# Kernel optimization log

Measured on AMD Instinct MI355X. Metric: run time of the kernel, lower is better.

## Reference

```python
import jax, jax.numpy as jnp
import numpy as np

N, D_IN, D_LAT, K = 200000, 256, 64, 100
ALPHA = 1000.0


def setup_inputs() -> dict:
    key = jax.random.key(0)
    k1, k2, k3, k4 = jax.random.split(key, 4)
    X = jax.random.normal(k1, (N, D_IN), dtype=jnp.float32)
    encoding = jax.random.normal(k2, (N, D_LAT), dtype=jnp.float32)
    decoding = jax.random.normal(k3, (N, D_IN), dtype=jnp.float32)
    # xavier_uniform bound for [K, D]: sqrt(6/(K+D))
    bound = np.sqrt(6.0 / (K + D_LAT)).astype(np.float32)
    centres = jax.random.uniform(k4, (K, D_LAT), dtype=jnp.float32,
                                 minval=-bound, maxval=bound)
    return {"X": X, "encoding": encoding, "decoding": decoding, "centres": centres}


def _cluster_kl(encoding, centres):
    # squared euclidean distances [N, K]
    d2 = (jnp.sum(encoding * encoding, axis=1, keepdims=True)
          + jnp.sum(centres * centres, axis=1)[None, :]
          - 2.0 * encoding @ centres.T)
    d2 = jnp.maximum(d2, 0.0)
    # Student-t (1 dof) soft assignment (DEC)
    q = 1.0 / (1.0 + d2)
    q = q / jnp.sum(q, axis=1, keepdims=True)          # [N, K]
    # target distribution p = (q^2 / f) normalized, detached
    f = jnp.sum(q, axis=0)                              # [K]
    p = (q * q) / f
    p = p / jnp.sum(p, axis=1, keepdims=True)
    p = jax.lax.stop_gradient(p)
    # F.kl_div(log q, p, reduction='batchmean') = sum p*(log p - log q) / N
    kl = jnp.sum(p * (jnp.log(p) - jnp.log(q))) / q.shape[0]
    return kl


def reference(X, encoding, decoding, centres):
    decoder_loss = jnp.mean((X - decoding) ** 2)
    cluster_loss = _cluster_kl(encoding, centres)
    return decoder_loss + cluster_loss * ALPHA
```

## Files before the change

### kernel.cpp

```cpp
#include <hip/hip_runtime.h>

#define N_ROWS 200000
#define D_IN   256
#define D_LAT  64
#define K_CL   100
#define NT     7
#define TPB    256

#define GRPS   3125
#define NMF    625
#define GPB    5

#define SC_HALF   3125
#define NSLOT     64

typedef __attribute__((ext_vector_type(8))) short bf16x8;
typedef __attribute__((ext_vector_type(4))) float f32x4;

__device__ __forceinline__ float rcpf(float x) { return __builtin_amdgcn_rcpf(x); }

__device__ __forceinline__ short f2bf(float f) {
    union { float f; unsigned u; } v; v.f = f;
    unsigned r = (v.u + 0x7fffu + ((v.u >> 16) & 1u)) >> 16;
    return (short)r;
}

__device__ __forceinline__ void cvt8r(float4 a, float4 b, bf16x8& o, float& sq) {
    sq = fmaf(a.x, a.x, sq); sq = fmaf(a.y, a.y, sq);
    sq = fmaf(a.z, a.z, sq); sq = fmaf(a.w, a.w, sq);
    sq = fmaf(b.x, b.x, sq); sq = fmaf(b.y, b.y, sq);
    sq = fmaf(b.z, b.z, sq); sq = fmaf(b.w, b.w, sq);
    o[0] = f2bf(a.x); o[1] = f2bf(a.y); o[2] = f2bf(a.z); o[3] = f2bf(a.w);
    o[4] = f2bf(b.x); o[5] = f2bf(b.y); o[6] = f2bf(b.z); o[7] = f2bf(b.w);
}

__device__ __forceinline__ void cvt8(const float* __restrict__ p, bf16x8& o, float& sq) {
    float4 a = *(const float4*)p;
    float4 b = *(const float4*)(p + 4);
    cvt8r(a, b, o, sq);
}

#define LANE_IDS()                                                             \
    const int tid = threadIdx.x;                                               \
    const int l   = tid & 63;                                                  \
    const int w   = tid >> 6;                                                  \
    const int c16 = l & 15;                                                    \
    const int g   = l >> 4;

#define PROLOGUE_B()                                                           \
    bf16x8 bfrag[NT][2];                                                       \
    float  cn2v[NT];                                                           \
    _Pragma("unroll")                                                          \
    for (int t = 0; t < NT; ++t) {                                             \
        int col = t * 16 + c16;                                                \
        bool valid = col < K_CL;                                               \
        float sq = 0.f;                                                        \
        _Pragma("unroll")                                                      \
        for (int kt = 0; kt < 2; ++kt) {                                       \
            bf16x8 bf;                                                         \
            if (valid) {                                                       \
                cvt8(cen + col * D_LAT + kt * 32 + g * 8, bf, sq);             \
            } else {                                                           \
                _Pragma("unroll")                                              \
                for (int i = 0; i < 8; ++i) bf[i] = 0;                         \
            }                                                                  \
            bfrag[t][kt] = bf;                                                 \
        }                                                                      \
        sq += __shfl_xor(sq, 16);                                              \
        sq += __shfl_xor(sq, 32);                                              \
        cn2v[t] = sq;                                                          \
    }                                                                          \
    const bool v6 = (c16 < 4);

#define LOADS4(grp, A)                                                         \
    {                                                                          \
        const int rowbase_ = (grp) * 64 + w * 16;                              \
        const float* arow_ = enc + (size_t)(rowbase_ + c16) * D_LAT + g * 8;   \
        A[0] = *(const float4*)(arow_);                                        \
        A[1] = *(const float4*)(arow_ + 4);                                    \
        A[2] = *(const float4*)(arow_ + 32);                                   \
        A[3] = *(const float4*)(arow_ + 36);                                   \
    }

#define GROUP_COMPUTE_FROM(A)                                                  \
    float en2p = 0.f;                                                          \
    bf16x8 afrag0, afrag1;                                                     \
    cvt8r(A[0], A[1], afrag0, en2p);                                           \
    cvt8r(A[2], A[3], afrag1, en2p);                                           \
    en2p += __shfl_xor(en2p, 16);                                              \
    en2p += __shfl_xor(en2p, 32);                                              \
    f32x4 acc[NT];                                                             \
    _Pragma("unroll")                                                          \
    for (int t = 0; t < NT; ++t) {                                             \
        acc[t][0] = 0.f; acc[t][1] = 0.f; acc[t][2] = 0.f; acc[t][3] = 0.f;    \
    }                                                                          \
    _Pragma("unroll")                                                          \
    for (int t = 0; t < NT; ++t)                                               \
        acc[t] = __builtin_amdgcn_mfma_f32_16x16x32_bf16(afrag0, bfrag[t][0], acc[t], 0, 0, 0); \
    _Pragma("unroll")                                                          \
    for (int t = 0; t < NT; ++t)                                               \
        acc[t] = __builtin_amdgcn_mfma_f32_16x16x32_bf16(afrag1, bfrag[t][1], acc[t], 0, 0, 0); \
    float en2r[4];                                                             \
    _Pragma("unroll")                                                          \
    for (int r = 0; r < 4; ++r) en2r[r] = __shfl(en2p, g * 4 + r);             \
    float qv[NT][4];                                                           \
    float rs[4] = {0.f, 0.f, 0.f, 0.f};                                        \
    _Pragma("unroll")                                                          \
    for (int t = 0; t < NT; ++t) {                                             \
        _Pragma("unroll")                                                      \
        for (int r = 0; r < 4; ++r) {                                          \
            float d2 = en2r[r] + cn2v[t] - 2.f * acc[t][r];                    \
            float q = rcpf(1.f + fmaxf(d2, 0.f));                              \
            if (t == 6 && !v6) q = 0.f;                                        \
            qv[t][r] = q; rs[r] += q;                                          \
        }                                                                      \
    }                                                                          \
    _Pragma("unroll")                                                          \
    for (int r = 0; r < 4; ++r) {                                              \
        rs[r] += __shfl_xor(rs[r], 1); rs[r] += __shfl_xor(rs[r], 2);          \
        rs[r] += __shfl_xor(rs[r], 4); rs[r] += __shfl_xor(rs[r], 8);          \
        rs[r] = rcpf(rs[r]);                                                   \
    }

__device__ __forceinline__ void dec_stream(const f32x4* __restrict__ X,
                                           const f32x4* __restrict__ Dec,
                                           double* __restrict__ slots,
                                           int cidx) {
    const int idx = cidx * 2048 + (int)threadIdx.x;
    f32x4 a[8], b[8];
#pragma unroll
    for (int u = 0; u < 8; ++u) a[u] = X[idx + u * 256];
#pragma unroll
    for (int u = 0; u < 8; ++u) b[u] = Dec[idx + u * 256];
    __builtin_amdgcn_sched_barrier(0);
    float local = 0.f;
#pragma unroll
    for (int u = 0; u < 8; ++u) {
        f32x4 d = a[u] - b[u];
        local = fmaf(d.x, d.x, local); local = fmaf(d.y, d.y, local);
        local = fmaf(d.z, d.z, local); local = fmaf(d.w, d.w, local);
    }
    local += __shfl_xor(local, 1);  local += __shfl_xor(local, 2);
    local += __shfl_xor(local, 4);  local += __shfl_xor(local, 8);
    local += __shfl_xor(local, 16); local += __shfl_xor(local, 32);
    if ((threadIdx.x & 63) == 0)
        atomicAdd(&slots[(cidx + (threadIdx.x >> 6)) & (NSLOT - 1)], (double)local);
}

__global__ void __launch_bounds__(TPB) k_d1(const f32x4* __restrict__ X,
                                            const f32x4* __restrict__ Xdec,
                                            const float* __restrict__ enc,
                                            const float* __restrict__ cen,
                                            double* __restrict__ dec_slots,
                                            float* __restrict__ fg) {
    if (blockIdx.x >= NMF) {
        dec_stream(X, Xdec, dec_slots, (int)blockIdx.x - NMF);
        return;
    }
    LANE_IDS();
    const int p1id = blockIdx.x;
    float4 abuf[2][4];
    LOADS4(p1id, abuf[0]);
    PROLOGUE_B();
    float facc[NT];
#pragma unroll
    for (int t = 0; t < NT; ++t) facc[t] = 0.f;
#pragma unroll
    for (int j = 0; j < GPB; ++j) {
        if (j + 1 < GPB) LOADS4(p1id + (j + 1) * NMF, abuf[(j + 1) & 1]);
        GROUP_COMPUTE_FROM(abuf[j & 1]);
#pragma unroll
        for (int t = 0; t < NT; ++t) {
            float a = 0.f;
#pragma unroll
            for (int r = 0; r < 4; ++r) a = fmaf(qv[t][r], rs[r], a);
            facc[t] += a;
        }
    }
    __shared__ float f_s[K_CL];
    for (int i = tid; i < K_CL; i += TPB) f_s[i] = 0.f;
    __syncthreads();
#pragma unroll
    for (int t = 0; t < NT; ++t) {
        float a = facc[t];
        a += __shfl_xor(a, 16);
        a += __shfl_xor(a, 32);
        int col = t * 16 + c16;
        if (g == 0 && col < K_CL) atomicAdd(&f_s[col], a);
    }
    __syncthreads();
    for (int i = tid; i < K_CL; i += TPB) atomicAdd(&fg[i], f_s[i]);
}

__global__ void __launch_bounds__(TPB) k_d2(const f32x4* __restrict__ X,
                                            const f32x4* __restrict__ Xdec,
                                            const float* __restrict__ enc,
                                            const float* __restrict__ cen,
                                            const float* __restrict__ fg,
                                            double* __restrict__ dec_slots,
                                            double* __restrict__ kl_slots) {
    if (blockIdx.x >= NMF) {
        dec_stream(X, Xdec, dec_slots, SC_HALF + (int)blockIdx.x - NMF);
        return;
    }
    LANE_IDS();
    const int p2id = blockIdx.x;
    float4 abuf[2][4];
    LOADS4(p2id, abuf[0]);
    PROLOGUE_B();
    float lfv[NT], rfv[NT];
#pragma unroll
    for (int t = 0; t < NT; ++t) {
        int col = t * 16 + c16;
        if (col < K_CL) {
            float fv = fg[col];
            lfv[t] = __logf(fv);
            rfv[t] = rcpf(fv);
        } else { lfv[t] = 0.f; rfv[t] = 0.f; }
    }
    float kl_local = 0.f;
#pragma unroll
    for (int j = 0; j < GPB; ++j) {
        if (j + 1 < GPB) LOADS4(p2id + (j + 1) * NMF, abuf[(j + 1) & 1]);
        GROUP_COMPUTE_FROM(abuf[j & 1]);
        float tac[4] = {0.f, 0.f, 0.f, 0.f};
        float Ap[4]  = {0.f, 0.f, 0.f, 0.f};
        float Bp[4]  = {0.f, 0.f, 0.f, 0.f};
#pragma unroll
        for (int t = 0; t < NT; ++t) {
#pragma unroll
            for (int r = 0; r < 4; ++r) {
                if (t == 6 && !v6) continue;
                float q = qv[t][r] * rs[r];
                float pu = q * q * rfv[t];
                tac[r] += pu;
                Ap[r] = fmaf(pu, __logf(q), Ap[r]);
                Bp[r] = fmaf(pu, lfv[t], Bp[r]);
            }
        }
#pragma unroll
        for (int r = 0; r < 4; ++r) {
            tac[r] += __shfl_xor(tac[r], 1); tac[r] += __shfl_xor(tac[r], 2);
            tac[r] += __shfl_xor(tac[r], 4); tac[r] += __shfl_xor(tac[r], 8);
            Ap[r]  += __shfl_xor(Ap[r], 1);  Ap[r]  += __shfl_xor(Ap[r], 2);
            Ap[r]  += __shfl_xor(Ap[r], 4);  Ap[r]  += __shfl_xor(Ap[r], 8);
            Bp[r]  += __shfl_xor(Bp[r], 1);  Bp[r]  += __shfl_xor(Bp[r], 2);
            Bp[r]  += __shfl_xor(Bp[r], 4);  Bp[r]  += __shfl_xor(Bp[r], 8);
        }
        if (c16 == 0) {
#pragma unroll
            for (int r = 0; r < 4; ++r)
                kl_local += (Ap[r] - Bp[r]) * rcpf(tac[r]) - __logf(tac[r]);
        }
    }
    __shared__ float red[TPB];
    red[tid] = kl_local;
    __syncthreads();
    for (int off = TPB / 2; off > 0; off >>= 1) {
        if (tid < off) red[tid] += red[tid + off];
        __syncthreads();
    }
    if (tid == 0) atomicAdd(&kl_slots[p2id & (NSLOT - 1)], (double)red[0]);
}

__global__ void k_final(const double* __restrict__ dec_s,
                        const double* __restrict__ kl_s,
                        float* __restrict__ out) {
    int l = threadIdx.x;
    double d = dec_s[l];
    double k = kl_s[l];
#pragma unroll
    for (int off = 32; off > 0; off >>= 1) {
        d += __shfl_xor(d, off);
        k += __shfl_xor(k, off);
    }
    if (l == 0)
        out[0] = (float)(d / ((double)N_ROWS * (double)D_IN) + 1000.0 * (k / (double)N_ROWS));
}

extern "C" void kernel_launch(void* const* d_in, const int* in_sizes, int n_in,
                              void* d_out, int out_size, void* d_ws, size_t ws_size,
                              hipStream_t stream) {
    (void)in_sizes; (void)n_in; (void)out_size; (void)ws_size;
    const float* X   = (const float*)d_in[0];
    const float* enc = (const float*)d_in[1];
    const float* dec = (const float*)d_in[2];
    const float* cen = (const float*)d_in[3];
    float* out = (float*)d_out;

    double* dec_slots = (double*)d_ws;
    double* kl_slots  = (double*)((char*)d_ws + 512);
    float*  fg        = (float*)((char*)d_ws + 1024);

    hipMemsetAsync(d_ws, 0, 1536, stream);
    k_d1<<<NMF + SC_HALF, TPB, 0, stream>>>(
        (const f32x4*)X, (const f32x4*)dec, enc, cen, dec_slots, fg);
    k_d2<<<NMF + SC_HALF, TPB, 0, stream>>>(
        (const f32x4*)X, (const f32x4*)dec, enc, cen, fg, dec_slots, kl_slots);
    k_final<<<1, 64, 0, stream>>>(dec_slots, kl_slots, out);
}
```

Baseline: 145.6 us.

## Turn decoder-loss stream into persistent double-buffered blocks with per-slot writes

```diff
diff --git a/kernel.cpp b/kernel.cpp
--- a/kernel.cpp
+++ b/kernel.cpp
@@ -11,8 +11,8 @@
 #define NMF    625
 #define GPB    5
 
-#define SC_HALF   3125
-#define NSLOT     64
+#define NCH    6250
+#define NSTR   1024
 
 typedef __attribute__((ext_vector_type(8))) short bf16x8;
 typedef __attribute__((ext_vector_type(4))) float f32x4;
@@ -125,26 +125,59 @@
 __device__ __forceinline__ void dec_stream(const f32x4* __restrict__ X,
                                            const f32x4* __restrict__ Dec,
                                            double* __restrict__ slots,
-                                           int cidx) {
-    const int idx = cidx * 2048 + (int)threadIdx.x;
-    f32x4 a[8], b[8];
-#pragma unroll
-    for (int u = 0; u < 8; ++u) a[u] = X[idx + u * 256];
-#pragma unroll
-    for (int u = 0; u < 8; ++u) b[u] = Dec[idx + u * 256];
-    __builtin_amdgcn_sched_barrier(0);
+                                           int sid, int cbase, int slotbase) {
+    const int tid = (int)threadIdx.x;
     float local = 0.f;
-#pragma unroll
-    for (int u = 0; u < 8; ++u) {
-        f32x4 d = a[u] - b[u];
-        local = fmaf(d.x, d.x, local); local = fmaf(d.y, d.y, local);
-        local = fmaf(d.z, d.z, local); local = fmaf(d.w, d.w, local);
+    f32x4 a0[4], b0[4], a1[4], b1[4];
+    int c = sid;
+    {
+        const int idx = (cbase + c) * 1024 + tid;
+#pragma unroll
+        for (int u = 0; u < 4; ++u) a0[u] = X[idx + u * 256];
+#pragma unroll
+        for (int u = 0; u < 4; ++u) b0[u] = Dec[idx + u * 256];
+    }
+#pragma unroll 1
+    while (true) {
+        const int c1 = c + NSTR;
+        if (c1 < NCH) {
+            const int idx1 = (cbase + c1) * 1024 + tid;
+#pragma unroll
+            for (int u = 0; u < 4; ++u) a1[u] = X[idx1 + u * 256];
+#pragma unroll
+            for (int u = 0; u < 4; ++u) b1[u] = Dec[idx1 + u * 256];
+        }
+        __builtin_amdgcn_sched_barrier(0);
+#pragma unroll
+        for (int u = 0; u < 4; ++u) {
+            f32x4 d = a0[u] - b0[u];
+            local = fmaf(d.x, d.x, local); local = fmaf(d.y, d.y, local);
+            local = fmaf(d.z, d.z, local); local = fmaf(d.w, d.w, local);
+        }
+        if (c1 >= NCH) break;
+        const int c2 = c1 + NSTR;
+        if (c2 < NCH) {
+            const int idx2 = (cbase + c2) * 1024 + tid;
+#pragma unroll
+            for (int u = 0; u < 4; ++u) a0[u] = X[idx2 + u * 256];
+#pragma unroll
+            for (int u = 0; u < 4; ++u) b0[u] = Dec[idx2 + u * 256];
+        }
+        __builtin_amdgcn_sched_barrier(0);
+#pragma unroll
+        for (int u = 0; u < 4; ++u) {
+            f32x4 d = a1[u] - b1[u];
+            local = fmaf(d.x, d.x, local); local = fmaf(d.y, d.y, local);
+            local = fmaf(d.z, d.z, local); local = fmaf(d.w, d.w, local);
+        }
+        if (c2 >= NCH) break;
+        c = c2;
     }
     local += __shfl_xor(local, 1);  local += __shfl_xor(local, 2);
     local += __shfl_xor(local, 4);  local += __shfl_xor(local, 8);
     local += __shfl_xor(local, 16); local += __shfl_xor(local, 32);
-    if ((threadIdx.x & 63) == 0)
-        atomicAdd(&slots[(cidx + (threadIdx.x >> 6)) & (NSLOT - 1)], (double)local);
+    if ((tid & 63) == 0)
+        slots[slotbase + sid * 4 + (tid >> 6)] = (double)local;
 }
 
 __global__ void __launch_bounds__(TPB) k_d1(const f32x4* __restrict__ X,
@@ -154,7 +187,7 @@
                                             double* __restrict__ dec_slots,
                                             float* __restrict__ fg) {
     if (blockIdx.x >= NMF) {
-        dec_stream(X, Xdec, dec_slots, (int)blockIdx.x - NMF);
+        dec_stream(X, Xdec, dec_slots, (int)blockIdx.x - NMF, 0, 0);
         return;
     }
     LANE_IDS();
@@ -200,7 +233,7 @@
                                             double* __restrict__ dec_slots,
                                             double* __restrict__ kl_slots) {
     if (blockIdx.x >= NMF) {
-        dec_stream(X, Xdec, dec_slots, SC_HALF + (int)blockIdx.x - NMF);
+        dec_stream(X, Xdec, dec_slots, (int)blockIdx.x - NMF, NCH, NSTR * 4);
         return;
     }
     LANE_IDS();
@@ -260,22 +293,26 @@
         if (tid < off) red[tid] += red[tid + off];
         __syncthreads();
     }
-    if (tid == 0) atomicAdd(&kl_slots[p2id & (NSLOT - 1)], (double)red[0]);
+    if (tid == 0) kl_slots[p2id] = (double)red[0];
 }
 
 __global__ void k_final(const double* __restrict__ dec_s,
                         const double* __restrict__ kl_s,
                         float* __restrict__ out) {
-    int l = threadIdx.x;
-    double d = dec_s[l];
-    double k = kl_s[l];
-#pragma unroll
-    for (int off = 32; off > 0; off >>= 1) {
-        d += __shfl_xor(d, off);
-        k += __shfl_xor(k, off);
-    }
-    if (l == 0)
-        out[0] = (float)(d / ((double)N_ROWS * (double)D_IN) + 1000.0 * (k / (double)N_ROWS));
+    __shared__ double rd[256], rk[256];
+    const int t = threadIdx.x;
+    double d = 0.0, k = 0.0;
+    for (int i = t; i < NSTR * 8; i += 256) d += dec_s[i];
+    for (int i = t; i < NMF; i += 256) k += kl_s[i];
+    rd[t] = d; rk[t] = k;
+    __syncthreads();
+    for (int off = 128; off > 0; off >>= 1) {
+        if (t < off) { rd[t] += rd[t + off]; rk[t] += rk[t + off]; }
+        __syncthreads();
+    }
+    if (t == 0)
+        out[0] = (float)(rd[0] / ((double)N_ROWS * (double)D_IN)
+                         + 1000.0 * (rk[0] / (double)N_ROWS));
 }
 
 extern "C" void kernel_launch(void* const* d_in, const int* in_sizes, int n_in,
@@ -289,13 +326,13 @@
     float* out = (float*)d_out;
 
     double* dec_slots = (double*)d_ws;
-    double* kl_slots  = (double*)((char*)d_ws + 512);
-    float*  fg        = (float*)((char*)d_ws + 1024);
-
-    hipMemsetAsync(d_ws, 0, 1536, stream);
-    k_d1<<<NMF + SC_HALF, TPB, 0, stream>>>(
+    double* kl_slots  = (double*)((char*)d_ws + 65536);
+    float*  fg        = (float*)((char*)d_ws + 73728);
+
+    hipMemsetAsync((char*)d_ws + 73728, 0, 512, stream);
+    k_d1<<<NMF + NSTR, TPB, 0, stream>>>(
         (const f32x4*)X, (const f32x4*)dec, enc, cen, dec_slots, fg);
-    k_d2<<<NMF + SC_HALF, TPB, 0, stream>>>(
+    k_d2<<<NMF + NSTR, TPB, 0, stream>>>(
         (const f32x4*)X, (const f32x4*)dec, enc, cen, fg, dec_slots, kl_slots);
-    k_final<<<1, 64, 0, stream>>>(dec_slots, kl_slots, out);
-}
+    k_final<<<1, 256, 0, stream>>>(dec_slots, kl_slots, out);
+}
```

After: 143.7 us. About the same (-1.3%).
